# Kernel optimization log

Hardware: AMD Instinct MI355X
Metric: run time of the kernel (lower is better)

Reference implementation:

```python
import jax, jax.numpy as jnp
import numpy as np

B, S, D = 2, 2048, 1024
H, HKV, HD = 16, 4, 64
FF = 4096
WINDOW = 1024
EPS = 1e-6


def _rope_tables(seq_len, head_dim, base=10000.0):
    inv_freq = 1.0 / (base ** (np.arange(0, head_dim, 2, dtype=np.float32) / head_dim))
    t = np.arange(seq_len, dtype=np.float32)
    freqs = np.outer(t, inv_freq)                       # [S, HD/2]
    emb = np.concatenate([freqs, freqs], axis=-1)       # [S, HD]
    return jnp.asarray(np.cos(emb)), jnp.asarray(np.sin(emb))


def setup_inputs() -> dict:
    key = jax.random.key(0)
    ks = jax.random.split(key, 16)
    s = lambda fan: 1.0 / np.sqrt(fan)
    cos, sin = _rope_tables(S, HD)
    return {
        "hidden_states": jax.random.normal(ks[0], (B, S, D), jnp.float32),
        "cos": cos, "sin": sin,
        "wq": jax.random.normal(ks[1], (D, H * HD), jnp.float32) * s(D),
        "bq": jnp.zeros((H * HD,), jnp.float32),
        "wk": jax.random.normal(ks[2], (D, HKV * HD), jnp.float32) * s(D),
        "bk": jnp.zeros((HKV * HD,), jnp.float32),
        "wv": jax.random.normal(ks[3], (D, HKV * HD), jnp.float32) * s(D),
        "bv": jnp.zeros((HKV * HD,), jnp.float32),
        "wo": jax.random.normal(ks[4], (H * HD, D), jnp.float32) * s(H * HD),
        "ln1_w": jnp.ones((D,), jnp.float32),
        "ln2_w": jnp.ones((D,), jnp.float32),
        "w_gate": jax.random.normal(ks[5], (D, FF), jnp.float32) * s(D),
        "w_up": jax.random.normal(ks[6], (D, FF), jnp.float32) * s(D),
        "w_down": jax.random.normal(ks[7], (FF, D), jnp.float32) * s(FF),
    }


def _rmsnorm(x, w, eps=EPS):
    var = jnp.mean(x.astype(jnp.float32) ** 2, axis=-1, keepdims=True)
    return (x * jax.lax.rsqrt(var + eps)).astype(x.dtype) * w


def _rotate_half(x):
    x1, x2 = jnp.split(x, 2, axis=-1)
    return jnp.concatenate([-x2, x1], axis=-1)


def reference(hidden_states, cos, sin, wq, bq, wk, bk, wv, bv, wo,
              ln1_w, ln2_w, w_gate, w_up, w_down):
    residual = hidden_states
    h = _rmsnorm(hidden_states, ln1_w)

    # projections -> [B, S, H, HD]
    q = (h @ wq + bq).reshape(B, S, H, HD)
    k = (h @ wk + bk).reshape(B, S, HKV, HD)
    v = (h @ wv + bv).reshape(B, S, HKV, HD)

    # RoPE
    c = cos[None, :, None, :]
    sn = sin[None, :, None, :]
    q = q * c + _rotate_half(q) * sn
    k = k * c + _rotate_half(k) * sn

    # GQA: repeat KV heads to H heads
    groups = H // HKV
    k = jnp.repeat(k, groups, axis=2)  # [B, S, H, HD]
    v = jnp.repeat(v, groups, axis=2)

    # sliding-window causal attention (flex_attention block-mask semantics)
    scale = 1.0 / np.sqrt(HD)
    scores = jnp.einsum("bqhd,bkhd->bhqk", q, k) * scale  # [B, H, S, S]
    i = jnp.arange(S)[:, None]
    j = jnp.arange(S)[None, :]
    mask = (j <= i) & (i - j < WINDOW)
    scores = jnp.where(mask[None, None], scores, jnp.finfo(scores.dtype).min)
    attn = jax.nn.softmax(scores, axis=-1)
    ctx = jnp.einsum("bhqk,bkhd->bqhd", attn, v).reshape(B, S, H * HD)

    h = residual + ctx @ wo

    residual2 = h
    h2 = _rmsnorm(h, ln2_w)
    mlp = (jax.nn.silu(h2 @ w_gate) * (h2 @ w_up)) @ w_down
    return residual2 + mlp
```

## Files before the change

### kernel.cpp

```cpp
#include <hip/hip_runtime.h>
#include <hip/hip_bf16.h>
#include <hip/hip_fp16.h>
#include <math.h>

#define BB 2
#define SS 2048
#define DD 1024
#define HH 16
#define HKVN 4
#define HDIM 64
#define FFD 4096
#define WND 1024
#define EPSF 1e-6f

typedef _Float16 f16;
typedef _Float16 half8 __attribute__((ext_vector_type(8)));
typedef float f32x4 __attribute__((ext_vector_type(4)));
typedef unsigned int u32;

#define GLOAD_LDS(gp, lp)                                                  \
  __builtin_amdgcn_global_load_lds(                                        \
      (const __attribute__((address_space(1))) u32*)(gp),                  \
      (__attribute__((address_space(3))) u32*)(lp), 16, 0, 0)

static __device__ inline u32 pack2(float a, float b) {
  unsigned short ua = __builtin_bit_cast(unsigned short, (f16)a);
  unsigned short ub = __builtin_bit_cast(unsigned short, (f16)b);
  return (u32)ua | ((u32)ub << 16);
}

__global__ __launch_bounds__(256) void prep_weights_kernel(
    const float* __restrict__ wq, const float* __restrict__ wk,
    const float* __restrict__ wv, const float* __restrict__ wo,
    const float* __restrict__ wg, const float* __restrict__ wu,
    const float* __restrict__ wd, const float* __restrict__ bq,
    const float* __restrict__ bk, const float* __restrict__ bv,
    f16* __restrict__ qkvT, f16* __restrict__ woT, f16* __restrict__ wgT,
    f16* __restrict__ wuT, f16* __restrict__ wdT, float* __restrict__ biasC) {
  int t = blockIdx.x;
  if (t >= 3712) {
    int i = (t - 3712) * 256 + threadIdx.x;
    if (i < 1024)
      biasC[i] = bq[i];
    else if (i < 1280)
      biasC[i] = bk[i - 1024];
    else if (i < 1536)
      biasC[i] = bv[i - 1280];
    return;
  }
  const float* W;
  f16* Wt;
  int K, N, lt;
  if (t < 256) {
    W = wq; Wt = qkvT; K = 1024; N = 1024; lt = t;
  } else if (t < 320) {
    W = wk; Wt = qkvT + (size_t)1024 * 1024; K = 1024; N = 256; lt = t - 256;
  } else if (t < 384) {
    W = wv; Wt = qkvT + (size_t)1280 * 1024; K = 1024; N = 256; lt = t - 320;
  } else if (t < 640) {
    W = wo; Wt = woT; K = 1024; N = 1024; lt = t - 384;
  } else if (t < 1664) {
    W = wg; Wt = wgT; K = 1024; N = 4096; lt = t - 640;
  } else if (t < 2688) {
    W = wu; Wt = wuT; K = 1024; N = 4096; lt = t - 1664;
  } else {
    W = wd; Wt = wdT; K = 4096; N = 1024; lt = t - 2688;
  }
  int ntx = N >> 6;
  int n0 = (lt % ntx) * 64, k0 = (lt / ntx) * 64;
  __shared__ float tile[64][65];
  int tx = threadIdx.x & 63, tr = threadIdx.x >> 6;
#pragma unroll
  for (int i = 0; i < 16; i++) {
    int r = tr + i * 4;
    tile[r][tx] = W[(size_t)(k0 + r) * N + n0 + tx];
  }
  __syncthreads();
  int kx = (threadIdx.x & 31) * 2;
  int rr = threadIdx.x >> 5;
#pragma unroll
  for (int i = 0; i < 8; i++) {
    int r = rr + i * 8;
    u32 w = pack2(tile[kx][r], tile[kx + 1][r]);
    *(u32*)(Wt + (size_t)(n0 + r) * K + k0 + kx) = w;
  }
}

__global__ __launch_bounds__(256) void rmsnorm_kernel(
    const float* __restrict__ x, const float* __restrict__ w,
    f16* __restrict__ out) {
  int row = blockIdx.x;
  int tid = threadIdx.x;
  float4 v = ((const float4*)(x + (size_t)row * 1024))[tid];
  float ss = v.x * v.x + v.y * v.y + v.z * v.z + v.w * v.w;
  for (int o = 32; o > 0; o >>= 1) ss += __shfl_down(ss, o, 64);
  __shared__ float red[4];
  int wid = tid >> 6, lane = tid & 63;
  if (lane == 0) red[wid] = ss;
  __syncthreads();
  if (tid == 0)
    red[0] = rsqrtf((red[0] + red[1] + red[2] + red[3]) / 1024.f + EPSF);
  __syncthreads();
  float rs = red[0];
  float4 wv = ((const float4*)w)[tid];
  u32 lo = pack2(v.x * rs * wv.x, v.y * rs * wv.y);
  u32 hi = pack2(v.z * rs * wv.z, v.w * rs * wv.w);
  *(int2*)(out + (size_t)row * 1024 + tid * 4) = make_int2((int)lo, (int)hi);
}

__global__ __launch_bounds__(256) void mfma_gemm(
    const f16* __restrict__ A, const f16* __restrict__ Bt,
    const float* __restrict__ bias, const float* __restrict__ resid,
    float* __restrict__ Cf, f16* __restrict__ Ch, int M, int N, int K) {
  __shared__ __align__(16) char smem[3 * 16384];
  const int tid = threadIdx.x;
  const int lane = tid & 63;
  const int wid = tid >> 6;
  const int wr = wid >> 1, wc = wid & 1;
  const int row0 = blockIdx.y * 128, col0 = blockIdx.x * 128;

  f32x4 acc[4][4];
#pragma unroll
  for (int m = 0; m < 4; m++)
#pragma unroll
    for (int n = 0; n < 4; n++) acc[m][n] = (f32x4){0.f, 0.f, 0.f, 0.f};

  auto stage = [&](int buf, int k0) {
    char* base = smem + buf * 16384;
#pragma unroll
    for (int q = 0; q < 2; q++) {
      int s = wid * 128 + q * 64 + lane;
      int r = s >> 2;
      int cg = (s & 3) ^ ((r >> 1) & 3);
      size_t goff = (size_t)r * K + k0 + cg * 8;
      u32 ldsb = (u32)((wid * 2 + q) * 1024);
      GLOAD_LDS(A + (size_t)row0 * K + goff, base + ldsb);
      GLOAD_LDS(Bt + (size_t)col0 * K + goff, base + 8192 + ldsb);
    }
  };
  auto off = [&](int r, int g) -> int {
    return r * 64 + ((g ^ ((r >> 1) & 3)) << 4);
  };

  const int nt = K / 32;
  stage(0, 0);
  if (nt > 1) stage(1, 32);
  int cur = 0;
  const int g = lane >> 4, l15 = lane & 15;
  for (int t = 0; t < nt; t++) {
    if (t + 1 < nt)
      asm volatile("s_waitcnt vmcnt(4)" ::: "memory");
    else
      asm volatile("s_waitcnt vmcnt(0)" ::: "memory");
    asm volatile("s_waitcnt lgkmcnt(0)" ::: "memory");
    __builtin_amdgcn_sched_barrier(0);
    __builtin_amdgcn_s_barrier();
    __builtin_amdgcn_sched_barrier(0);
    const char* base = smem + cur * 16384;
    half8 af[4], bf[4];
#pragma unroll
    for (int m = 0; m < 4; m++) {
      int r = wr * 64 + m * 16 + l15;
      af[m] = *(const half8*)(base + off(r, g));
    }
#pragma unroll
    for (int n = 0; n < 4; n++) {
      int c = wc * 64 + n * 16 + l15;
      bf[n] = *(const half8*)(base + 8192 + off(c, g));
    }
    if (t + 2 < nt) {
      int nb = cur + 2;
      if (nb >= 3) nb -= 3;
      stage(nb, (t + 2) * 32);
    }
    __builtin_amdgcn_s_setprio(1);
#pragma unroll
    for (int m = 0; m < 4; m++)
#pragma unroll
      for (int n = 0; n < 4; n++)
        acc[m][n] =
            __builtin_amdgcn_mfma_f32_16x16x32_f16(af[m], bf[n], acc[m][n], 0, 0, 0);
    __builtin_amdgcn_s_setprio(0);
    cur = (cur + 1 == 3) ? 0 : cur + 1;
  }

#pragma unroll
  for (int m = 0; m < 4; m++) {
#pragma unroll
    for (int n = 0; n < 4; n++) {
#pragma unroll
      for (int v = 0; v < 4; v++) {
        int r = row0 + wr * 64 + m * 16 + (lane >> 4) * 4 + v;
        int c = col0 + wc * 64 + n * 16 + l15;
        float vv = acc[m][n][v];
        if (bias) vv += bias[c];
        if (Ch) {
          Ch[(size_t)r * N + c] = (f16)vv;
        } else {
          if (resid) vv += resid[(size_t)r * N + c];
          Cf[(size_t)r * N + c] = vv;
        }
      }
    }
  }
}

__global__ __launch_bounds__(512) void gateup_gemm(
    const f16* __restrict__ A, const f16* __restrict__ Wg,
    const f16* __restrict__ Wu, f16* __restrict__ ACT, int M, int N, int K) {
  __shared__ __align__(16) char smem[3 * 40960];
  const int tid = threadIdx.x;
  const int lane = tid & 63;
  const int wid = tid >> 6;
  const int wr = wid >> 2;
  const int wc = wid & 3;
  const int row0 = blockIdx.y * 128, col0 = blockIdx.x * 256;

  f32x4 accg[4][4], accu[4][4];
#pragma unroll
  for (int m = 0; m < 4; m++)
#pragma unroll
    for (int n = 0; n < 4; n++) {
      accg[m][n] = (f32x4){0.f, 0.f, 0.f, 0.f};
      accu[m][n] = (f32x4){0.f, 0.f, 0.f, 0.f};
    }

  auto stage = [&](int buf, int k0) {
    char* base = smem + buf * 40960;
    {
      int s = tid;
      int r = s >> 2;
      int cg = (s & 3) ^ ((r >> 1) & 3);
      size_t goff = (size_t)r * K + k0 + cg * 8;
      GLOAD_LDS(A + (size_t)row0 * K + goff, base + wid * 1024);
    }
#pragma unroll
    for (int p = 0; p < 2; p++) {
      int s = p * 512 + tid;
      int r = s >> 2;
      int cg = (s & 3) ^ ((r >> 1) & 3);
      size_t goff = (size_t)r * K + k0 + cg * 8;
      GLOAD_LDS(Wg + (size_t)col0 * K + goff,
                base + 8192 + p * 8192 + wid * 1024);
    }
#pragma unroll
    for (int p = 0; p < 2; p++) {
      int s = p * 512 + tid;
      int r = s >> 2;
      int cg = (s & 3) ^ ((r >> 1) & 3);
      size_t goff = (size_t)r * K + k0 + cg * 8;
      GLOAD_LDS(Wu + (size_t)col0 * K + goff,
                base + 24576 + p * 8192 + wid * 1024);
    }
  };
  auto off = [&](int r, int g) -> int {
    return r * 64 + ((g ^ ((r >> 1) & 3)) << 4);
  };

  const int nt = K / 32;
  stage(0, 0);
  if (nt > 1) stage(1, 32);
  int cur = 0;
  const int g = lane >> 4, l15 = lane & 15;
  for (int t = 0; t < nt; t++) {
    if (t + 1 < nt)
      asm volatile("s_waitcnt vmcnt(5)" ::: "memory");
    else
      asm volatile("s_waitcnt vmcnt(0)" ::: "memory");
    asm volatile("s_waitcnt lgkmcnt(0)" ::: "memory");
    __builtin_amdgcn_sched_barrier(0);
    __builtin_amdgcn_s_barrier();
    __builtin_amdgcn_sched_barrier(0);
    const char* base = smem + cur * 40960;
    half8 af[4], gf[4], uf[4];
#pragma unroll
    for (int m = 0; m < 4; m++) {
      int r = wr * 64 + m * 16 + l15;
      af[m] = *(const half8*)(base + off(r, g));
    }
#pragma unroll
    for (int n = 0; n < 4; n++) {
      int c = wc * 64 + n * 16 + l15;
      gf[n] = *(const half8*)(base + 8192 + off(c, g));
      uf[n] = *(const half8*)(base + 24576 + off(c, g));
    }
    if (t + 2 < nt) {
      int nb = cur + 2;
      if (nb >= 3) nb -= 3;
      stage(nb, (t + 2) * 32);
    }
    __builtin_amdgcn_s_setprio(1);
#pragma unroll
    for (int m = 0; m < 4; m++)
#pragma unroll
      for (int n = 0; n < 4; n++) {
        accg[m][n] =
            __builtin_amdgcn_mfma_f32_16x16x32_f16(af[m], gf[n], accg[m][n], 0, 0, 0);
        accu[m][n] =
            __builtin_amdgcn_mfma_f32_16x16x32_f16(af[m], uf[n], accu[m][n], 0, 0, 0);
      }
    __builtin_amdgcn_s_setprio(0);
    cur = (cur + 1 == 3) ? 0 : cur + 1;
  }

#pragma unroll
  for (int m = 0; m < 4; m++) {
#pragma unroll
    for (int n = 0; n < 4; n++) {
#pragma unroll
      for (int v = 0; v < 4; v++) {
        int r = row0 + wr * 64 + m * 16 + (lane >> 4) * 4 + v;
        int c = col0 + wc * 64 + n * 16 + l15;
        float gg = accg[m][n][v];
        float uu = accu[m][n][v];
        float sv = gg / (1.f + __expf(-gg));
        ACT[(size_t)r * N + c] = (f16)(sv * uu);
      }
    }
  }
}

__global__ __launch_bounds__(256) void rope_cast_kernel(
    const f16* __restrict__ QKV, const float* __restrict__ cos_t,
    const float* __restrict__ sin_t, f16* __restrict__ Qh,
    f16* __restrict__ Kh) {
  int idx = blockIdx.x * blockDim.x + threadIdx.x;
  int d = idx & 31;
  int rest = idx >> 5;
  int head = rest % (HH + HKVN);
  int bs = rest / (HH + HKVN);
  int s = bs % SS;
  float c = cos_t[s * HDIM + d];
  float sn = sin_t[s * HDIM + d];
  const f16* rowp = QKV + (size_t)bs * 1536;
  if (head < HH) {
    const f16* base = rowp + head * HDIM;
    float x1 = (float)base[d], x2 = (float)base[d + 32];
    f16* ob = Qh + ((size_t)bs * HH + head) * HDIM;
    ob[d] = (f16)((x1 * c - x2 * sn) * 0.125f);
    ob[d + 32] = (f16)((x2 * c + x1 * sn) * 0.125f);
  } else {
    int hk = head - HH;
    const f16* base = rowp + 1024 + hk * HDIM;
    float x1 = (float)base[d], x2 = (float)base[d + 32];
    f16* ob = Kh + ((size_t)bs * HKVN + hk) * HDIM;
    ob[d] = (f16)(x1 * c - x2 * sn);
    ob[d + 32] = (f16)(x2 * c + x1 * sn);
  }
}

__global__ __launch_bounds__(256) void vtrans_kernel(
    const f16* __restrict__ QKV, f16* __restrict__ Vt) {
  __shared__ f16 tile[64][72];
  int st = blockIdx.x & 31;
  int hk = (blockIdx.x >> 5) & 3;
  int b = blockIdx.x >> 7;
  int s0 = st * 64;
  int tid = threadIdx.x;
  int r = tid >> 2, cg = tid & 3;
#pragma unroll
  for (int i = 0; i < 2; i++) {
    const f16* src = QKV + (size_t)(b * SS + s0 + r) * 1536 + 1280 + hk * HDIM +
                     cg * 16 + i * 8;
    *(int4*)&tile[r][cg * 16 + i * 8] = *(const int4*)src;
  }
  __syncthreads();
  int dd = tid >> 2, sg = tid & 3;
#pragma unroll
  for (int i = 0; i < 4; i++) {
    int c0 = sg * 16 + i * 4;
    unsigned short a0 = __builtin_bit_cast(unsigned short, tile[c0 + 0][dd]);
    unsigned short a1 = __builtin_bit_cast(unsigned short, tile[c0 + 1][dd]);
    unsigned short a2 = __builtin_bit_cast(unsigned short, tile[c0 + 2][dd]);
    unsigned short a3 = __builtin_bit_cast(unsigned short, tile[c0 + 3][dd]);
    u32 w0 = (u32)a0 | ((u32)a1 << 16);
    u32 w1 = (u32)a2 | ((u32)a3 << 16);
    *(int2*)(Vt + ((size_t)(b * HKVN + hk) * HDIM + dd) * SS + s0 + c0) =
        make_int2((int)w0, (int)w1);
  }
}

__global__ __launch_bounds__(256) void attn_kernel(
    const f16* __restrict__ Qh, const f16* __restrict__ Kh,
    const f16* __restrict__ Vt, f16* __restrict__ O) {
  __shared__ __align__(16) char smem[2 * 16384 + 4 * 4608];
  const int tid = threadIdx.x;
  const int lane = tid & 63;
  const int wid = tid >> 6;
  const int l15 = lane & 15;
  const int g = lane >> 4;
  int qt = blockIdx.x & 63;
  int hk = (blockIdx.x >> 6) & 3;
  int b = blockIdx.x >> 8;
  int s0 = qt * 32;
  int h = hk * 4 + wid;

  half8 qf[2][2];
#pragma unroll
  for (int n = 0; n < 2; n++) {
    int q = s0 + n * 16 + l15;
    const f16* qp = Qh + (((size_t)b * SS + q) * HH + h) * HDIM;
#pragma unroll
    for (int kk = 0; kk < 2; kk++) qf[n][kk] = *(const half8*)(qp + kk * 32 + g * 8);
  }

  const int tb = (s0 >= WND) ? ((s0 - (WND - 1)) >> 6) : 0;
  const int te = (s0 + 31) >> 6;

  f32x4 acc_o[2][4];
#pragma unroll
  for (int m2 = 0; m2 < 2; m2++)
#pragma unroll
    for (int n = 0; n < 4; n++) acc_o[m2][n] = (f32x4){0.f, 0.f, 0.f, 0.f};
  float mrun[2] = {-1e30f, -1e30f};
  float lrun[2] = {0.f, 0.f};

  char* pw = smem + 32768 + wid * 4608;

  auto stage = [&](int buf, int tt) {
    int jt0 = tt * 64;
    char* kbase = smem + buf * 16384;
#pragma unroll
    for (int q2 = 0; q2 < 2; q2++) {
      int slot = (wid * 2 + q2) * 64 + lane;
      int r = slot >> 3, c = slot & 7;
      int cc = c ^ (r & 7);
      u32 ldsb = (u32)((wid * 2 + q2) * 1024);
      const f16* gk =
          Kh + ((size_t)(b * SS + jt0 + r) * HKVN + hk) * HDIM + cc * 8;
      GLOAD_LDS(gk, kbase + ldsb);
      const f16* gv =
          Vt + ((size_t)(b * HKVN + hk) * HDIM + r) * SS + jt0 + cc * 8;
      GLOAD_LDS(gv, kbase + 8192 + ldsb);
    }
  };

  stage(0, tb);
  __syncthreads();
  for (int tt = tb; tt <= te; tt++) {
    int buf = (tt - tb) & 1;
    if (tt < te) stage(buf ^ 1, tt + 1);
    const char* kb = smem + buf * 16384;
    const char* vbp = kb + 8192;
    int jt0 = tt * 64;

    f32x4 acc_s[4][2];
#pragma unroll
    for (int m = 0; m < 4; m++)
#pragma unroll
      for (int n = 0; n < 2; n++) acc_s[m][n] = (f32x4){0.f, 0.f, 0.f, 0.f};
#pragma unroll
    for (int kk = 0; kk < 2; kk++) {
      half8 af[4];
#pragma unroll
      for (int m = 0; m < 4; m++) {
        int key = m * 16 + l15;
        af[m] = *(const half8*)(kb + key * 128 + (((kk * 4 + g) ^ (key & 7)) << 4));
      }
#pragma unroll
      for (int m = 0; m < 4; m++)
#pragma unroll
        for (int n = 0; n < 2; n++)
          acc_s[m][n] = __builtin_amdgcn_mfma_f32_16x16x32_f16(af[m], qf[n][kk],
                                                               acc_s[m][n], 0, 0, 0);
    }

    float tmax[2] = {-1e38f, -1e38f};
#pragma unroll
    for (int m = 0; m < 4; m++)
#pragma unroll
      for (int n = 0; n < 2; n++)
#pragma unroll
        for (int v = 0; v < 4; v++) {
          int j = jt0 + m * 16 + g * 4 + v;
          int q = s0 + n * 16 + l15;
          float s = acc_s[m][n][v];
          s = ((unsigned)(q - j) < (unsigned)WND) ? s : -1e38f;
          acc_s[m][n][v] = s;
          tmax[n] = fmaxf(tmax[n], s);
        }
#pragma unroll
    for (int n = 0; n < 2; n++) {
      tmax[n] = fmaxf(tmax[n], __shfl_xor(tmax[n], 16, 64));
      tmax[n] = fmaxf(tmax[n], __shfl_xor(tmax[n], 32, 64));
    }
    float corr[2], rs[2];
#pragma unroll
    for (int n = 0; n < 2; n++) {
      float mn = fmaxf(mrun[n], tmax[n]);
      corr[n] = __expf(mrun[n] - mn);
      mrun[n] = mn;
      rs[n] = 0.f;
    }
#pragma unroll
    for (int m = 0; m < 4; m++)
#pragma unroll
      for (int n = 0; n < 2; n++) {
        float p0 = __expf(acc_s[m][n][0] - mrun[n]);
        float p1 = __expf(acc_s[m][n][1] - mrun[n]);
        float p2 = __expf(acc_s[m][n][2] - mrun[n]);
        float p3 = __expf(acc_s[m][n][3] - mrun[n]);
        rs[n] += (p0 + p1) + (p2 + p3);
        *(int2*)(pw + (n * 16 + l15) * 144 + (m * 16 + g * 4) * 2) =
            make_int2((int)pack2(p0, p1), (int)pack2(p2, p3));
      }
#pragma unroll
    for (int n = 0; n < 2; n++) {
      rs[n] += __shfl_xor(rs[n], 16, 64);
      rs[n] += __shfl_xor(rs[n], 32, 64);
      lrun[n] = lrun[n] * corr[n] + rs[n];
    }
#pragma unroll
    for (int m2 = 0; m2 < 2; m2++)
#pragma unroll
      for (int v = 0; v < 4; v++) {
        float cw = __shfl(corr[m2], g * 4 + v, 64);
#pragma unroll
        for (int n = 0; n < 4; n++) acc_o[m2][n][v] *= cw;
      }
#pragma unroll
    for (int kk = 0; kk < 2; kk++) {
      half8 ap[2], vf[4];
#pragma unroll
      for (int m2 = 0; m2 < 2; m2++)
        ap[m2] = *(const half8*)(pw + (m2 * 16 + l15) * 144 + (kk * 32 + g * 8) * 2);
#pragma unroll
      for (int n = 0; n < 4; n++) {
        int d = n * 16 + l15;
        vf[n] = *(const half8*)(vbp + d * 128 + (((kk * 4 + g) ^ (d & 7)) << 4));
      }
#pragma unroll
      for (int m2 = 0; m2 < 2; m2++)
#pragma unroll
        for (int n = 0; n < 4; n++)
          acc_o[m2][n] = __builtin_amdgcn_mfma_f32_16x16x32_f16(ap[m2], vf[n],
                                                                acc_o[m2][n], 0, 0, 0);
    }
    __syncthreads();
  }

#pragma unroll
  for (int m2 = 0; m2 < 2; m2++)
#pragma unroll
    for (int v = 0; v < 4; v++) {
      float li = __shfl(lrun[m2], g * 4 + v, 64);
      float inv = 1.f / li;
      int q = s0 + m2 * 16 + g * 4 + v;
#pragma unroll
      for (int n = 0; n < 4; n++) {
        int d = n * 16 + l15;
        O[(((size_t)b * SS + q) * HH + h) * HDIM + d] =
            (f16)(acc_o[m2][n][v] * inv);
      }
    }
}

extern "C" void kernel_launch(void* const* d_in, const int* in_sizes, int n_in,
                              void* d_out, int out_size, void* d_ws,
                              size_t ws_size, hipStream_t stream) {
  const float* hidden = (const float*)d_in[0];
  const float* cos_t = (const float*)d_in[1];
  const float* sin_t = (const float*)d_in[2];
  const float* wq = (const float*)d_in[3];
  const float* bq = (const float*)d_in[4];
  const float* wk = (const float*)d_in[5];
  const float* bk = (const float*)d_in[6];
  const float* wv = (const float*)d_in[7];
  const float* bv = (const float*)d_in[8];
  const float* wo = (const float*)d_in[9];
  const float* ln1 = (const float*)d_in[10];
  const float* ln2 = (const float*)d_in[11];
  const float* wg = (const float*)d_in[12];
  const float* wu = (const float*)d_in[13];
  const float* wd = (const float*)d_in[14];
  float* out = (float*)d_out;
  char* ws = (char*)d_ws;

  const int M = BB * SS;

  f16* qkvT = (f16*)ws;
  f16* woT = (f16*)(ws + (3u << 20));
  f16* wgT = (f16*)(ws + (5u << 20));
  f16* wuT = (f16*)(ws + (13u << 20));
  f16* wdT = (f16*)(ws + (21u << 20));
  f16* Anh = (f16*)(ws + (29u << 20));
  f16* CTXh = (f16*)(ws + (37u << 20));
  f16* QKVh = (f16*)(ws + (45u << 20));
  f16* Qh = (f16*)(ws + (57u << 20));
  f16* Kh = (f16*)(ws + (65u << 20));
  f16* Vt = (f16*)(ws + (67u << 20));
  f16* ACTh = (f16*)(ws + (45u << 20));
  float* biasC = (float*)(ws + (81u << 20));

  prep_weights_kernel<<<3718, 256, 0, stream>>>(wq, wk, wv, wo, wg, wu, wd, bq,
                                                bk, bv, qkvT, woT, wgT, wuT,
                                                wdT, biasC);
  rmsnorm_kernel<<<M, 256, 0, stream>>>(hidden, ln1, Anh);
  mfma_gemm<<<dim3(1536 / 128, M / 128), 256, 0, stream>>>(
      Anh, qkvT, biasC, nullptr, nullptr, QKVh, M, 1536, DD);
  rope_cast_kernel<<<(BB * SS * (HH + HKVN) * 32) / 256, 256, 0, stream>>>(
      QKVh, cos_t, sin_t, Qh, Kh);
  vtrans_kernel<<<BB * HKVN * (SS / 64), 256, 0, stream>>>(QKVh, Vt);
  attn_kernel<<<BB * HKVN * (SS / 32), 256, 0, stream>>>(Qh, Kh, Vt, CTXh);
  mfma_gemm<<<dim3(DD / 128, M / 128), 256, 0, stream>>>(
      CTXh, woT, nullptr, hidden, out, nullptr, M, DD, DD);
  rmsnorm_kernel<<<M, 256, 0, stream>>>(out, ln2, Anh);
  gateup_gemm<<<dim3(FFD / 256, M / 128), 512, 0, stream>>>(Anh, wgT, wuT, ACTh,
                                                            M, FFD, DD);
  mfma_gemm<<<dim3(DD / 128, M / 128), 256, 0, stream>>>(
      ACTh, wdT, nullptr, out, out, nullptr, M, DD, FFD);
}
```

Baseline: 276.4 us.

## Fuse RoPE into QKV GEMM epilogue and use 64-wide tiles for N=1024 GEMMs

The QKV projection GEMM now applies bias, RoPE and the Q scale in its epilogue and writes Q, K and a compact V buffer directly. This removes the separate rope_cast kernel and the round trip of the full QKV intermediate through memory. The output-projection and down-projection GEMMs switch to a new 128x64-tile kernel, which doubles the block count for N=1024 and should fill more compute units. The trade-off is less data reuse per block and scattered epilogue stores.

```diff
diff --git a/kernel.cpp b/kernel.cpp
--- a/kernel.cpp
+++ b/kernel.cpp
@@ -108,10 +108,11 @@
   *(int2*)(out + (size_t)row * 1024 + tid * 4) = make_int2((int)lo, (int)hi);
 }
 
-__global__ __launch_bounds__(256) void mfma_gemm(
+__global__ __launch_bounds__(256) void qkv_gemm(
     const f16* __restrict__ A, const f16* __restrict__ Bt,
-    const float* __restrict__ bias, const float* __restrict__ resid,
-    float* __restrict__ Cf, f16* __restrict__ Ch, int M, int N, int K) {
+    const float* __restrict__ biasC, const float* __restrict__ cos_t,
+    const float* __restrict__ sin_t, f16* __restrict__ Qh,
+    f16* __restrict__ Kh, f16* __restrict__ Vh, int M, int N, int K) {
   __shared__ __align__(16) char smem[3 * 16384];
   const int tid = threadIdx.x;
   const int lane = tid & 63;
@@ -184,22 +185,139 @@
     cur = (cur + 1 == 3) ? 0 : cur + 1;
   }
 
+  const int typ = (col0 < 1024) ? 0 : (col0 < 1280 ? 1 : 2);
 #pragma unroll
   for (int m = 0; m < 4; m++) {
 #pragma unroll
-    for (int n = 0; n < 4; n++) {
+    for (int v = 0; v < 4; v++) {
+      int r = row0 + wr * 64 + m * 16 + (lane >> 4) * 4 + v;
+      int s = r & (SS - 1);
+      if (typ == 2) {
+#pragma unroll
+        for (int n = 0; n < 4; n++) {
+          int c = col0 + wc * 64 + n * 16 + l15;
+          float vv = acc[m][n][v] + biasC[c];
+          Vh[(size_t)r * 256 + (c - 1280)] = (f16)vv;
+        }
+      } else {
+#pragma unroll
+        for (int n = 0; n < 2; n++) {
+          int d = n * 16 + l15;
+          int c1 = col0 + wc * 64 + d;
+          float x1 = acc[m][n][v] + biasC[c1];
+          float x2 = acc[m][n + 2][v] + biasC[c1 + 32];
+          float cv = cos_t[s * HDIM + d];
+          float sv = sin_t[s * HDIM + d];
+          float o1 = x1 * cv - x2 * sv;
+          float o2 = x2 * cv + x1 * sv;
+          if (typ == 0) {
+            int h = c1 >> 6;
+            f16* qp = Qh + ((size_t)r * HH + h) * HDIM + d;
+            qp[0] = (f16)(o1 * 0.125f);
+            qp[32] = (f16)(o2 * 0.125f);
+          } else {
+            int hk = (c1 - 1024) >> 6;
+            f16* kp = Kh + ((size_t)r * HKVN + hk) * HDIM + d;
+            kp[0] = (f16)o1;
+            kp[32] = (f16)o2;
+          }
+        }
+      }
+    }
+  }
+}
+
+__global__ __launch_bounds__(256) void gemm_n64(
+    const f16* __restrict__ A, const f16* __restrict__ Bt,
+    const float* __restrict__ resid, float* __restrict__ Cf, int M, int N,
+    int K) {
+  __shared__ __align__(16) char smem[3 * 12288];
+  const int tid = threadIdx.x;
+  const int lane = tid & 63;
+  const int wid = tid >> 6;
+  const int wr = wid >> 1, wc = wid & 1;
+  const int row0 = blockIdx.y * 128, col0 = blockIdx.x * 64;
+
+  f32x4 acc[4][2];
+#pragma unroll
+  for (int m = 0; m < 4; m++)
+#pragma unroll
+    for (int n = 0; n < 2; n++) acc[m][n] = (f32x4){0.f, 0.f, 0.f, 0.f};
+
+  auto stage = [&](int buf, int k0) {
+    char* base = smem + buf * 12288;
+#pragma unroll
+    for (int p = 0; p < 2; p++) {
+      int s = p * 256 + tid;
+      int r = s >> 2;
+      int cg = (s & 3) ^ ((r >> 1) & 3);
+      size_t goff = (size_t)r * K + k0 + cg * 8;
+      GLOAD_LDS(A + (size_t)row0 * K + goff, base + p * 4096 + wid * 1024);
+    }
+    {
+      int s = tid;
+      int r = s >> 2;
+      int cg = (s & 3) ^ ((r >> 1) & 3);
+      size_t goff = (size_t)r * K + k0 + cg * 8;
+      GLOAD_LDS(Bt + (size_t)col0 * K + goff, base + 8192 + wid * 1024);
+    }
+  };
+  auto off = [&](int r, int g) -> int {
+    return r * 64 + ((g ^ ((r >> 1) & 3)) << 4);
+  };
+
+  const int nt = K / 32;
+  stage(0, 0);
+  if (nt > 1) stage(1, 32);
+  int cur = 0;
+  const int g = lane >> 4, l15 = lane & 15;
+  for (int t = 0; t < nt; t++) {
+    if (t + 1 < nt)
+      asm volatile("s_waitcnt vmcnt(3)" ::: "memory");
+    else
+      asm volatile("s_waitcnt vmcnt(0)" ::: "memory");
+    asm volatile("s_waitcnt lgkmcnt(0)" ::: "memory");
+    __builtin_amdgcn_sched_barrier(0);
+    __builtin_amdgcn_s_barrier();
+    __builtin_amdgcn_sched_barrier(0);
+    const char* base = smem + cur * 12288;
+    half8 af[4], bf[2];
+#pragma unroll
+    for (int m = 0; m < 4; m++) {
+      int r = wr * 64 + m * 16 + l15;
+      af[m] = *(const half8*)(base + off(r, g));
+    }
+#pragma unroll
+    for (int n = 0; n < 2; n++) {
+      int c = wc * 32 + n * 16 + l15;
+      bf[n] = *(const half8*)(base + 8192 + off(c, g));
+    }
+    if (t + 2 < nt) {
+      int nb = cur + 2;
+      if (nb >= 3) nb -= 3;
+      stage(nb, (t + 2) * 32);
+    }
+    __builtin_amdgcn_s_setprio(1);
+#pragma unroll
+    for (int m = 0; m < 4; m++)
+#pragma unroll
+      for (int n = 0; n < 2; n++)
+        acc[m][n] =
+            __builtin_amdgcn_mfma_f32_16x16x32_f16(af[m], bf[n], acc[m][n], 0, 0, 0);
+    __builtin_amdgcn_s_setprio(0);
+    cur = (cur + 1 == 3) ? 0 : cur + 1;
+  }
+
+#pragma unroll
+  for (int m = 0; m < 4; m++) {
+#pragma unroll
+    for (int n = 0; n < 2; n++) {
 #pragma unroll
       for (int v = 0; v < 4; v++) {
         int r = row0 + wr * 64 + m * 16 + (lane >> 4) * 4 + v;
-        int c = col0 + wc * 64 + n * 16 + l15;
-        float vv = acc[m][n][v];
-        if (bias) vv += bias[c];
-        if (Ch) {
-          Ch[(size_t)r * N + c] = (f16)vv;
-        } else {
-          if (resid) vv += resid[(size_t)r * N + c];
-          Cf[(size_t)r * N + c] = vv;
-        }
+        int c = col0 + wc * 32 + n * 16 + l15;
+        float vv = acc[m][n][v] + resid[(size_t)r * N + c];
+        Cf[(size_t)r * N + c] = vv;
       }
     }
   }
@@ -320,37 +438,8 @@
   }
 }
 
-__global__ __launch_bounds__(256) void rope_cast_kernel(
-    const f16* __restrict__ QKV, const float* __restrict__ cos_t,
-    const float* __restrict__ sin_t, f16* __restrict__ Qh,
-    f16* __restrict__ Kh) {
-  int idx = blockIdx.x * blockDim.x + threadIdx.x;
-  int d = idx & 31;
-  int rest = idx >> 5;
-  int head = rest % (HH + HKVN);
-  int bs = rest / (HH + HKVN);
-  int s = bs % SS;
-  float c = cos_t[s * HDIM + d];
-  float sn = sin_t[s * HDIM + d];
-  const f16* rowp = QKV + (size_t)bs * 1536;
-  if (head < HH) {
-    const f16* base = rowp + head * HDIM;
-    float x1 = (float)base[d], x2 = (float)base[d + 32];
-    f16* ob = Qh + ((size_t)bs * HH + head) * HDIM;
-    ob[d] = (f16)((x1 * c - x2 * sn) * 0.125f);
-    ob[d + 32] = (f16)((x2 * c + x1 * sn) * 0.125f);
-  } else {
-    int hk = head - HH;
-    const f16* base = rowp + 1024 + hk * HDIM;
-    float x1 = (float)base[d], x2 = (float)base[d + 32];
-    f16* ob = Kh + ((size_t)bs * HKVN + hk) * HDIM;
-    ob[d] = (f16)(x1 * c - x2 * sn);
-    ob[d + 32] = (f16)(x2 * c + x1 * sn);
-  }
-}
-
 __global__ __launch_bounds__(256) void vtrans_kernel(
-    const f16* __restrict__ QKV, f16* __restrict__ Vt) {
+    const f16* __restrict__ Vh, f16* __restrict__ Vt) {
   __shared__ f16 tile[64][72];
   int st = blockIdx.x & 31;
   int hk = (blockIdx.x >> 5) & 3;
@@ -360,8 +449,8 @@
   int r = tid >> 2, cg = tid & 3;
 #pragma unroll
   for (int i = 0; i < 2; i++) {
-    const f16* src = QKV + (size_t)(b * SS + s0 + r) * 1536 + 1280 + hk * HDIM +
-                     cg * 16 + i * 8;
+    const f16* src =
+        Vh + (size_t)(b * SS + s0 + r) * 256 + hk * HDIM + cg * 16 + i * 8;
     *(int4*)&tile[r][cg * 16 + i * 8] = *(const int4*)src;
   }
   __syncthreads();
@@ -585,7 +674,7 @@
   f16* wdT = (f16*)(ws + (21u << 20));
   f16* Anh = (f16*)(ws + (29u << 20));
   f16* CTXh = (f16*)(ws + (37u << 20));
-  f16* QKVh = (f16*)(ws + (45u << 20));
+  f16* Vh = (f16*)(ws + (45u << 20));
   f16* Qh = (f16*)(ws + (57u << 20));
   f16* Kh = (f16*)(ws + (65u << 20));
   f16* Vt = (f16*)(ws + (67u << 20));
@@ -596,17 +685,15 @@
                                                 bk, bv, qkvT, woT, wgT, wuT,
                                                 wdT, biasC);
   rmsnorm_kernel<<<M, 256, 0, stream>>>(hidden, ln1, Anh);
-  mfma_gemm<<<dim3(1536 / 128, M / 128), 256, 0, stream>>>(
-      Anh, qkvT, biasC, nullptr, nullptr, QKVh, M, 1536, DD);
-  rope_cast_kernel<<<(BB * SS * (HH + HKVN) * 32) / 256, 256, 0, stream>>>(
-      QKVh, cos_t, sin_t, Qh, Kh);
-  vtrans_kernel<<<BB * HKVN * (SS / 64), 256, 0, stream>>>(QKVh, Vt);
+  qkv_gemm<<<dim3(1536 / 128, M / 128), 256, 0, stream>>>(
+      Anh, qkvT, biasC, cos_t, sin_t, Qh, Kh, Vh, M, 1536, DD);
+  vtrans_kernel<<<BB * HKVN * (SS / 64), 256, 0, stream>>>(Vh, Vt);
   attn_kernel<<<BB * HKVN * (SS / 32), 256, 0, stream>>>(Qh, Kh, Vt, CTXh);
-  mfma_gemm<<<dim3(DD / 128, M / 128), 256, 0, stream>>>(
-      CTXh, woT, nullptr, hidden, out, nullptr, M, DD, DD);
+  gemm_n64<<<dim3(DD / 64, M / 128), 256, 0, stream>>>(CTXh, woT, hidden, out,
+                                                       M, DD, DD);
   rmsnorm_kernel<<<M, 256, 0, stream>>>(out, ln2, Anh);
   gateup_gemm<<<dim3(FFD / 256, M / 128), 512, 0, stream>>>(Anh, wgT, wuT, ACTh,
                                                             M, FFD, DD);
-  mfma_gemm<<<dim3(DD / 128, M / 128), 256, 0, stream>>>(
-      ACTh, wdT, nullptr, out, out, nullptr, M, DD, FFD);
-}
+  gemm_n64<<<dim3(DD / 64, M / 128), 256, 0, stream>>>(ACTh, wdT, out, out, M,
+                                                       DD, FFD);
+}
```

Measured after the change: 253.0 us. 8.5% less time.
